# Kernel optimization log

Measured on AMD Instinct MI355X. Metric: run time of the kernel, lower is better.

## Reference

```python
import jax, jax.numpy as jnp
import numpy as np

NC, NB, NT = 512, 128, 256   # feats dims: [channels, batch, time]
H = 512                      # hidden_size
NCLS = 97                    # num_classes
NUM_STEPS = 32               # fixed decode length (= text_length.max())


def setup_inputs() -> dict:
    key = jax.random.key(0)
    ks = jax.random.split(key, 12)
    s = 1.0 / np.sqrt(H)
    inp = {
        "feats": jax.random.normal(ks[0], (NC, NB, NT), jnp.float32),
        "text_length": jnp.full((NB,), NUM_STEPS, jnp.int32),
        # AttentionCell params
        "Wi2h": jax.random.normal(ks[1], (H, NC), jnp.float32) * s,   # i2h, no bias
        "Wh2h": jax.random.normal(ks[2], (H, H), jnp.float32) * s,
        "bh2h": jax.random.normal(ks[3], (H,), jnp.float32) * s,
        "Wscore": jax.random.normal(ks[4], (1, H), jnp.float32) * s,  # score, no bias
        # GRUCell params (gate order: r, z, n as in PyTorch)
        "Wih": jax.random.normal(ks[5], (3 * H, NC), jnp.float32) * s,
        "Whh": jax.random.normal(ks[6], (3 * H, H), jnp.float32) * s,
        "bih": jax.random.normal(ks[7], (3 * H,), jnp.float32) * s,
        "bhh": jax.random.normal(ks[8], (3 * H,), jnp.float32) * s,
        # generator: Linear(hidden_size, num_classes - 1)
        "Wgen": jax.random.normal(ks[9], (NCLS - 1, H), jnp.float32) * s,
        "bgen": jax.random.normal(ks[10], (NCLS - 1,), jnp.float32) * s,
    }
    return inp


def reference(feats, text_length, Wi2h, Wh2h, bh2h, Wscore, Wih, Whh, bih, bhh, Wgen, bgen):
    # feats: [nC, nB, nT]
    nC, nB, nT = feats.shape
    # i2h(feats) is step-independent -> hoist out of the loop (same math)
    feats_proj = jnp.einsum('cbt,hc->bth', feats, Wi2h)  # [nB, nT, H]
    w_score = Wscore[0]                                   # [H]

    def step(h, _):
        # additive attention
        hp = h @ Wh2h.T + bh2h                                  # [nB, H]
        e = jnp.tanh(feats_proj + hp[:, None, :]) @ w_score     # [nB, nT]
        alpha = jax.nn.softmax(e, axis=1)                       # [nB, nT]
        context = jnp.einsum('cbt,bt->bc', feats, alpha)        # [nB, nC]
        # GRUCell(context, h), PyTorch semantics
        gi = context @ Wih.T + bih                              # [nB, 3H]
        gh = h @ Whh.T + bhh                                    # [nB, 3H]
        ir, iz, in_ = jnp.split(gi, 3, axis=1)
        hr, hz, hn = jnp.split(gh, 3, axis=1)
        r = jax.nn.sigmoid(ir + hr)
        z = jax.nn.sigmoid(iz + hz)
        n = jnp.tanh(in_ + r * hn)
        h_new = (1.0 - z) * n + z * h
        return h_new, h_new

    h0 = jnp.zeros((nB, feats_proj.shape[-1]), feats.dtype)
    _, hiddens = jax.lax.scan(step, h0, None, length=NUM_STEPS)  # [T, nB, H]
    # all lengths == NUM_STEPS -> gather is a per-batch flatten
    new_hiddens = hiddens.transpose(1, 0, 2).reshape(-1, hiddens.shape[-1])  # [nB*T, H]
    probs = new_hiddens @ Wgen.T + bgen                          # [nB*T, NCLS-1]
    return probs
```

## Files before the change

kernel.cpp:

```cpp
#include <hip/hip_runtime.h>
#include <math.h>

#define NBATCH 128
#define NTIME  256
#define NCH    512
#define NH     512
#define NSTEPS 32
#define NOUT   96
#define MTOT   32768

typedef __attribute__((ext_vector_type(8))) short short8v;
typedef __attribute__((ext_vector_type(4))) float f32x4;

__device__ __forceinline__ float fast_tanh(float x) {
    x = fminf(fmaxf(x, -30.f), 30.f);
    float u = __expf(2.f * x);
    return (u - 1.f) / (u + 1.f);
}
__device__ __forceinline__ float fast_sigmoid(float x) {
    x = fminf(fmaxf(x, -30.f), 30.f);
    return 1.f / (1.f + __expf(-x));
}
__device__ __forceinline__ float wave_reduce_sum(float s) {
    #pragma unroll
    for (int off = 32; off; off >>= 1) s += __shfl_xor(s, off, 64);
    return s;
}
__device__ __forceinline__ float wave_reduce_max(float s) {
    #pragma unroll
    for (int off = 32; off; off >>= 1) s = fmaxf(s, __shfl_xor(s, off, 64));
    return s;
}
__device__ __forceinline__ unsigned short f2bf(float f) {
    unsigned u = __builtin_bit_cast(unsigned, f);
    return (unsigned short)((u + 0x7FFFu + ((u >> 16) & 1u)) >> 16);
}
__device__ __forceinline__ float bflo(unsigned u) {
    return __builtin_bit_cast(float, u << 16);
}
__device__ __forceinline__ float bfhi(unsigned u) {
    return __builtin_bit_cast(float, u & 0xFFFF0000u);
}

__global__ __launch_bounds__(256) void k_w2bf(const float* __restrict__ W,
                                              unsigned short* __restrict__ Wb) {
    #pragma unroll
    for (int r = 0; r < 4; ++r) {
        int idx = (blockIdx.x * 256 + threadIdx.x) + r * 16384;
        float4 v = *(const float4*)(W + (size_t)idx * 4);
        ushort4 o;
        o.x = f2bf(v.x); o.y = f2bf(v.y); o.z = f2bf(v.z); o.w = f2bf(v.w);
        *(ushort4*)(Wb + (size_t)idx * 4) = o;
    }
}

__global__ __launch_bounds__(256) void k_wg2bf(const float* __restrict__ Wih,
                                               const float* __restrict__ Whh,
                                               unsigned short* __restrict__ Wgb) {
    #pragma unroll
    for (int r = 0; r < 4; ++r) {
        int idx = (blockIdx.x * 256 + threadIdx.x) + r * 98304;
        const float* src = (idx < 196608) ? (Wih + (size_t)idx * 4)
                                          : (Whh + (size_t)(idx - 196608) * 4);
        float4 v = *(const float4*)src;
        ushort4 o;
        o.x = f2bf(v.x); o.y = f2bf(v.y); o.z = f2bf(v.z); o.w = f2bf(v.w);
        *(ushort4*)(Wgb + (size_t)idx * 4) = o;
    }
}

__global__ __launch_bounds__(256) void k_feats2bf(const float* __restrict__ feats,
                                                  unsigned short* __restrict__ Fb) {
    __shared__ float tl[64][65];
    const int m0 = (blockIdx.x & 511) * 64;
    const int k0 = (blockIdx.x >> 9) * 64;
    const int tid = threadIdx.x;
    #pragma unroll
    for (int p = 0; p < 4; ++p) {
        int fid = tid + p * 256;
        int row = fid >> 4, c4 = fid & 15;
        float4 v = *(const float4*)(feats + (size_t)(k0 + row) * MTOT + m0 + c4 * 4);
        tl[row][c4 * 4 + 0] = v.x; tl[row][c4 * 4 + 1] = v.y;
        tl[row][c4 * 4 + 2] = v.z; tl[row][c4 * 4 + 3] = v.w;
    }
    __syncthreads();
    #pragma unroll
    for (int p = 0; p < 4; ++p) {
        int cid = tid + p * 256;
        int mm = cid >> 4, ch = cid & 15;
        ushort4 o;
        o.x = f2bf(tl[ch * 4 + 0][mm]);
        o.y = f2bf(tl[ch * 4 + 1][mm]);
        o.z = f2bf(tl[ch * 4 + 2][mm]);
        o.w = f2bf(tl[ch * 4 + 3][mm]);
        *(ushort4*)(Fb + (size_t)(m0 + mm) * 512 + k0 + ch * 4) = o;
    }
}

__global__ __launch_bounds__(1024) void k_fcopy(const float* __restrict__ f,
                                                unsigned short* __restrict__ o) {
    int gid = blockIdx.x * 1024 + threadIdx.x;
    float4 v = *(const float4*)(f + (size_t)gid * 4);
    ushort4 s;
    s.x = f2bf(v.x); s.y = f2bf(v.y); s.z = f2bf(v.z); s.w = f2bf(v.w);
    *(ushort4*)(o + (size_t)gid * 4) = s;
}

__global__ __launch_bounds__(256) void k_fp_mfma(const unsigned short* __restrict__ Wb,
                                                 const unsigned short* __restrict__ Fb,
                                                 unsigned short* __restrict__ fp_bf) {
    __shared__ char SB[49152];
    unsigned short* As = (unsigned short*)SB;
    unsigned short* Bs = (unsigned short*)(SB + 16384);
    float* tl = (float*)SB;
    const int m0 = (blockIdx.x & 127) * 256;
    const int h0 = (blockIdx.x >> 7) * 128;
    const int tid = threadIdx.x;
    const int lane = tid & 63, wid = tid >> 6;
    const int wh = wid & 1, wm = wid >> 1;
    f32x4 acc[4][8];
    #pragma unroll
    for (int i = 0; i < 4; ++i)
        #pragma unroll
        for (int j = 0; j < 8; ++j) acc[i][j] = (f32x4)0.f;

    for (int k0 = 0; k0 < 512; k0 += 64) {
        #pragma unroll
        for (int i = 0; i < 4; ++i) {
            int cid = tid + i * 256;
            int row = cid >> 3, ch = cid & 7;
            uint4 v = *(const uint4*)(Wb + (size_t)(h0 + row) * 512 + k0 + ch * 8);
            *(uint4*)(As + row * 64 + ((ch ^ (row & 7)) << 3)) = v;
        }
        #pragma unroll
        for (int i = 0; i < 8; ++i) {
            int cid = tid + i * 256;
            int row = cid >> 3, ch = cid & 7;
            uint4 v = *(const uint4*)(Fb + (size_t)(m0 + row) * 512 + k0 + ch * 8);
            *(uint4*)(Bs + row * 64 + ((ch ^ (row & 7)) << 3)) = v;
        }
        __syncthreads();
        #pragma unroll
        for (int ks = 0; ks < 2; ++ks) {
            short8v a[4], b[8];
            #pragma unroll
            for (int hf = 0; hf < 4; ++hf) {
                int row = wh * 64 + hf * 16 + (lane & 15);
                int ch = ks * 4 + (lane >> 4);
                a[hf] = *(const short8v*)(As + row * 64 + ((ch ^ (row & 7)) << 3));
            }
            #pragma unroll
            for (int mf = 0; mf < 8; ++mf) {
                int row = wm * 128 + mf * 16 + (lane & 15);
                int ch = ks * 4 + (lane >> 4);
                b[mf] = *(const short8v*)(Bs + row * 64 + ((ch ^ (row & 7)) << 3));
            }
            #pragma unroll
            for (int hf = 0; hf < 4; ++hf)
                #pragma unroll
                for (int mf = 0; mf < 8; ++mf)
                    acc[hf][mf] = __builtin_amdgcn_mfma_f32_16x16x32_bf16(
                        a[hf], b[mf], acc[hf][mf], 0, 0, 0);
        }
        __syncthreads();
    }
    #pragma unroll
    for (int hf = 0; hf < 4; ++hf) {
        #pragma unroll
        for (int mf = 0; mf < 8; ++mf) {
            int ml = wm * 128 + mf * 16 + (lane & 15);
            int col = wh * 16 + (lane >> 4) * 4;
            tl[ml * 33 + col + 0] = acc[hf][mf][0];
            tl[ml * 33 + col + 1] = acc[hf][mf][1];
            tl[ml * 33 + col + 2] = acc[hf][mf][2];
            tl[ml * 33 + col + 3] = acc[hf][mf][3];
        }
        __syncthreads();
        #pragma unroll
        for (int mi = 0; mi < 8; ++mi) {
            int ml = (tid >> 3) + mi * 32;
            int hl4 = (tid & 7) * 4;
            float v0 = tl[ml * 33 + hl4 + 0];
            float v1 = tl[ml * 33 + hl4 + 1];
            float v2 = tl[ml * 33 + hl4 + 2];
            float v3 = tl[ml * 33 + hl4 + 3];
            int hg = h0 + ((hl4 < 16) ? (hf * 16 + hl4) : (64 + hf * 16 + hl4 - 16));
            ushort4 o;
            o.x = f2bf(v0); o.y = f2bf(v1); o.z = f2bf(v2); o.w = f2bf(v3);
            *(ushort4*)(fp_bf + (size_t)(m0 + ml) * 512 + hg) = o;
        }
        __syncthreads();
    }
}

__global__ __launch_bounds__(256) void k_wt(const float* __restrict__ W,
                                            unsigned short* __restrict__ WTb) {
    __shared__ float tl[32][33];
    const int bi = blockIdx.x & 15, bj = blockIdx.x >> 4;
    const int tx = threadIdx.x & 31, ty8 = threadIdx.x >> 5;
    #pragma unroll
    for (int i = 0; i < 4; ++i) {
        int r = ty8 * 4 + i;
        tl[r][tx] = W[(size_t)(bj * 32 + r) * NH + bi * 32 + tx];
    }
    __syncthreads();
    #pragma unroll
    for (int i = 0; i < 4; ++i) {
        int c = ty8 * 4 + i;
        WTb[(size_t)(bi * 32 + c) * NH + bj * 32 + tx] = f2bf(tl[tx][c]);
    }
}

__global__ __launch_bounds__(1024) void k_hp0(const float* __restrict__ bh2h,
                                              float* __restrict__ hp) {
    int i = blockIdx.x * 1024 + threadIdx.x;
    hp[i] = bh2h[i & 511];
}

__global__ __launch_bounds__(512) void k_e(const unsigned short* __restrict__ fp_bf,
                                           const float* __restrict__ hp,
                                           const float* __restrict__ wscore,
                                           float* __restrict__ e) {
    const int b = blockIdx.x >> 3;
    const int t0 = (blockIdx.x & 7) * 32;
    const int tid = threadIdx.x;
    const int lane = tid & 63, w = tid >> 6;
    float4 h0 = *(const float4*)(hp + (size_t)b * NH + lane * 8);
    float4 h1 = *(const float4*)(hp + (size_t)b * NH + lane * 8 + 4);
    float4 w0 = *(const float4*)(wscore + lane * 8);
    float4 w1 = *(const float4*)(wscore + lane * 8 + 4);
    const unsigned short* base = fp_bf + (size_t)(b * NTIME + t0 + w * 4) * NH + lane * 8;
    uint4 v0 = *(const uint4*)(base);
    uint4 v1 = *(const uint4*)(base + NH);
    uint4 v2 = *(const uint4*)(base + 2 * NH);
    uint4 v3 = *(const uint4*)(base + 3 * NH);
    uint4 vv[4] = {v0, v1, v2, v3};
    #pragma unroll
    for (int it = 0; it < 4; ++it) {
        uint4 v = vv[it];
        float s = fast_tanh(bflo(v.x) + h0.x) * w0.x + fast_tanh(bfhi(v.x) + h0.y) * w0.y +
                  fast_tanh(bflo(v.y) + h0.z) * w0.z + fast_tanh(bfhi(v.y) + h0.w) * w0.w +
                  fast_tanh(bflo(v.z) + h1.x) * w1.x + fast_tanh(bfhi(v.z) + h1.y) * w1.y +
                  fast_tanh(bflo(v.w) + h1.z) * w1.z + fast_tanh(bfhi(v.w) + h1.w) * w1.w;
        s = wave_reduce_sum(s);
        if (lane == 0) e[b * NTIME + t0 + w * 4 + it] = s;
    }
}

__global__ __launch_bounds__(512) void k_ctx2(const float* __restrict__ e,
                                              const unsigned short* __restrict__ featsb,
                                              unsigned short* __restrict__ ctx_bf) {
    __shared__ float als[256];
    __shared__ float red[8];
    const int b = blockIdx.x >> 3;
    const int c0 = (blockIdx.x & 7) * 64;
    const int tid = threadIdx.x;
    const int lane = tid & 63, w = tid >> 6;
    float v = (tid < 256) ? e[b * NTIME + tid] : -3.4e38f;
    float m = wave_reduce_max(v);
    if (lane == 0) red[w] = m;
    __syncthreads();
    m = red[0];
    #pragma unroll
    for (int i = 1; i < 8; ++i) m = fmaxf(m, red[i]);
    float ex = (tid < 256) ? __expf(v - m) : 0.f;
    float s = wave_reduce_sum(ex);
    __syncthreads();
    if (lane == 0) red[w] = s;
    __syncthreads();
    s = 0.f;
    #pragma unroll
    for (int i = 0; i < 8; ++i) s += red[i];
    if (tid < 256) als[tid] = ex / s;
    __syncthreads();

    float4 al = *(const float4*)&als[lane * 4];
    #pragma unroll
    for (int cc = 0; cc < 8; ++cc) {
        int c = c0 + w * 8 + cc;
        uint2 fv = *(const uint2*)(featsb + (size_t)(c * NBATCH + b) * NTIME + lane * 4);
        float sc = bflo(fv.x) * al.x + bfhi(fv.x) * al.y +
                   bflo(fv.y) * al.z + bfhi(fv.y) * al.w;
        sc = wave_reduce_sum(sc);
        if (lane == 0) ctx_bf[(size_t)b * NCH + c] = f2bf(sc);
    }
}

__global__ __launch_bounds__(256) void k_gmfma(const unsigned short* __restrict__ ctx_bf,
                                               const unsigned short* __restrict__ h_bf,
                                               const unsigned short* __restrict__ Wgb,
                                               float* __restrict__ g2) {
    __shared__ unsigned short As[128 * 64];
    __shared__ unsigned short Bs[128 * 64];
    const int j0 = blockIdx.x * 128;
    const unsigned short* A = (j0 < 1536) ? ctx_bf : h_bf;
    const int tid = threadIdx.x;
    const int lane = tid & 63, wid = tid >> 6;
    const int wb = wid & 1, wj = wid >> 1;
    f32x4 acc[4][4];
    #pragma unroll
    for (int i = 0; i < 4; ++i)
        #pragma unroll
        for (int j = 0; j < 4; ++j) acc[i][j] = (f32x4)0.f;

    for (int k0 = 0; k0 < 512; k0 += 64) {
        #pragma unroll
        for (int i = 0; i < 4; ++i) {
            int cid = tid + i * 256;
            int row = cid >> 3, ch = cid & 7;
            uint4 va = *(const uint4*)(A + (size_t)row * 512 + k0 + ch * 8);
            *(uint4*)(As + row * 64 + ((ch ^ (row & 7)) << 3)) = va;
            uint4 vb = *(const uint4*)(Wgb + (size_t)(j0 + row) * 512 + k0 + ch * 8);
            *(uint4*)(Bs + row * 64 + ((ch ^ (row & 7)) << 3)) = vb;
        }
        __syncthreads();
        #pragma unroll
        for (int ks = 0; ks < 2; ++ks) {
            short8v a[4], b[4];
            #pragma unroll
            for (int f = 0; f < 4; ++f) {
                int rowa = wb * 64 + f * 16 + (lane & 15);
                int rowb = wj * 64 + f * 16 + (lane & 15);
                int ch = ks * 4 + (lane >> 4);
                a[f] = *(const short8v*)(As + rowa * 64 + ((ch ^ (rowa & 7)) << 3));
                b[f] = *(const short8v*)(Bs + rowb * 64 + ((ch ^ (rowb & 7)) << 3));
            }
            #pragma unroll
            for (int bf = 0; bf < 4; ++bf)
                #pragma unroll
                for (int jf = 0; jf < 4; ++jf)
                    acc[bf][jf] = __builtin_amdgcn_mfma_f32_16x16x32_bf16(
                        a[bf], b[jf], acc[bf][jf], 0, 0, 0);
        }
        __syncthreads();
    }
    #pragma unroll
    for (int bf = 0; bf < 4; ++bf) {
        int b = wb * 64 + bf * 16 + (lane >> 4) * 4;
        #pragma unroll
        for (int jf = 0; jf < 4; ++jf) {
            int j = j0 + wj * 64 + jf * 16 + (lane & 15);
            *(f32x4*)(g2 + (size_t)j * NBATCH + b) = acc[bf][jf];
        }
    }
}

__global__ __launch_bounds__(1024) void k_comb_hp(const float* __restrict__ g2,
                                                  const float* __restrict__ hprev,
                                                  float* __restrict__ hidn,
                                                  unsigned short* __restrict__ h_bf,
                                                  const float* __restrict__ bih,
                                                  const float* __restrict__ bhh,
                                                  const unsigned short* __restrict__ WTb,
                                                  const float* __restrict__ bh2h,
                                                  float* __restrict__ hp) {
    __shared__ float h_s[4 * 512];
    __shared__ float scr2[16 * 4 * 16 * 4];
    const int blk = blockIdx.x;
    const int b0 = (blk >> 3) * 4;
    const int jbase = (blk & 7) * 64;
    const int tid = threadIdx.x;
    #pragma unroll
    for (int rep = 0; rep < 2; ++rep) {
        int idx = tid + rep * 1024;
        int bi = idx & 3, kk = idx >> 2;
        int b = b0 + bi;
        float ir  = g2[(size_t)(0 * 512 + kk) * NBATCH + b] + bih[kk];
        float iz  = g2[(size_t)(1 * 512 + kk) * NBATCH + b] + bih[512 + kk];
        float in_ = g2[(size_t)(2 * 512 + kk) * NBATCH + b] + bih[1024 + kk];
        float hr  = g2[(size_t)(3 * 512 + kk) * NBATCH + b] + bhh[kk];
        float hz  = g2[(size_t)(4 * 512 + kk) * NBATCH + b] + bhh[512 + kk];
        float hn  = g2[(size_t)(5 * 512 + kk) * NBATCH + b] + bhh[1024 + kk];
        float r = fast_sigmoid(ir + hr);
        float z = fast_sigmoid(iz + hz);
        float ng = fast_tanh(in_ + r * hn);
        float hv = hprev[(size_t)b * NH + kk];
        float hnew = (1.f - z) * ng + z * hv;
        h_s[bi * 512 + kk] = hnew;
        if ((blk & 7) == 0) {
            hidn[(size_t)b * NH + kk] = hnew;
            h_bf[(size_t)b * NH + kk] = f2bf(hnew);
        }
    }
    __syncthreads();
    {
        const int jq = tid & 15, bi = (tid >> 4) & 3, kq = tid >> 6;
        const int j = jbase + jq * 4;
        float4 acc = make_float4(0.f, 0.f, 0.f, 0.f);
        #pragma unroll 8
        for (int kk = 0; kk < 32; ++kk) {
            int k = kq * 32 + kk;
            uint2 wq = *(const uint2*)(WTb + (size_t)k * NH + j);
            float hv = h_s[bi * 512 + k];
            acc.x += hv * bflo(wq.x); acc.y += hv * bfhi(wq.x);
            acc.z += hv * bflo(wq.y); acc.w += hv * bfhi(wq.y);
        }
        *(float4*)&scr2[((kq * 4 + bi) * 16 + jq) * 4] = acc;
    }
    __syncthreads();
    if (tid < 64) {
        const int bi = tid >> 4, jq = tid & 15;
        float4 sum = make_float4(0.f, 0.f, 0.f, 0.f);
        #pragma unroll
        for (int kq = 0; kq < 16; ++kq) {
            float4 p = *(const float4*)&scr2[((kq * 4 + bi) * 16 + jq) * 4];
            sum.x += p.x; sum.y += p.y; sum.z += p.z; sum.w += p.w;
        }
        int j = jbase + jq * 4;
        float4 bb = *(const float4*)(bh2h + j);
        sum.x += bb.x; sum.y += bb.y; sum.z += bb.z; sum.w += bb.w;
        *(float4*)(hp + (size_t)(b0 + bi) * NH + j) = sum;
    }
}

__global__ __launch_bounds__(256) void k_gen(const float* __restrict__ hid,
                                             const float* __restrict__ Wgen,
                                             const float* __restrict__ bgen,
                                             float* __restrict__ out) {
    __shared__ float As[32][36];
    __shared__ float Bs[32][97];
    const int m0 = blockIdx.x * 32;
    const int tid = threadIdx.x;
    const int tx = tid & 31, ty = tid >> 5;
    float acc[4][3] = {};
    for (int k0 = 0; k0 < 512; k0 += 32) {
        {
            int mm = tid >> 3, kq = (tid & 7) << 2;
            int m = m0 + mm, s = m & 31, b = m >> 5;
            float4 v = *(const float4*)(hid + (size_t)(s + 1) * 65536 + b * 512 + k0 + kq);
            *(float4*)(&As[mm][kq]) = v;
        }
        #pragma unroll
        for (int i = 0; i < 3; ++i) {
            int f4 = tid + i * 256;
            int nn = f4 >> 3, kq = (f4 & 7) << 2;
            float4 v = *(const float4*)(Wgen + (size_t)nn * 512 + k0 + kq);
            Bs[kq + 0][nn] = v.x; Bs[kq + 1][nn] = v.y;
            Bs[kq + 2][nn] = v.z; Bs[kq + 3][nn] = v.w;
        }
        __syncthreads();
        #pragma unroll
        for (int kk = 0; kk < 32; ++kk) {
            float bv[3];
            #pragma unroll
            for (int j = 0; j < 3; ++j) bv[j] = Bs[kk][tx * 3 + j];
            #pragma unroll
            for (int i = 0; i < 4; ++i) {
                float a = As[ty * 4 + i][kk];
                #pragma unroll
                for (int j = 0; j < 3; ++j) acc[i][j] += a * bv[j];
            }
        }
        __syncthreads();
    }
    #pragma unroll
    for (int i = 0; i < 4; ++i)
        #pragma unroll
        for (int j = 0; j < 3; ++j)
            out[(size_t)(m0 + ty * 4 + i) * NOUT + tx * 3 + j] = acc[i][j] + bgen[tx * 3 + j];
}

extern "C" void kernel_launch(void* const* d_in, const int* in_sizes, int n_in,
                              void* d_out, int out_size, void* d_ws, size_t ws_size,
                              hipStream_t stream) {
    const float* feats  = (const float*)d_in[0];
    const float* Wi2h   = (const float*)d_in[2];
    const float* Wh2h   = (const float*)d_in[3];
    const float* bh2h   = (const float*)d_in[4];
    const float* Wscore = (const float*)d_in[5];
    const float* Wih    = (const float*)d_in[6];
    const float* Whh    = (const float*)d_in[7];
    const float* bih    = (const float*)d_in[8];
    const float* bhh    = (const float*)d_in[9];
    const float* Wgen   = (const float*)d_in[10];
    const float* bgen   = (const float*)d_in[11];
    float* out = (float*)d_out;

    float* ws  = (float*)d_ws;
    unsigned short* fp_bf  = (unsigned short*)ws;
    float*          hid    = ws + 8388608;
    float*          hpctx  = hid + 2162688;
    unsigned short* ctx_bf = (unsigned short*)(hpctx + 65536);
    unsigned short* h_bf   = (unsigned short*)(hpctx + 65536 + 32768);
    unsigned short* WTb    = (unsigned short*)(hpctx + 65536 + 65536);
    unsigned short* Wgb    = (unsigned short*)(hpctx + 65536 + 65536 + 131072);
    unsigned short* Wb     = (unsigned short*)(hpctx + 65536 + 65536 + 131072 + 786432);
    unsigned short* Fb     = (unsigned short*)(hpctx + 65536 + 65536 + 131072 + 786432 + 131072);
    unsigned short* featsb = Fb;

    float* e  = out;
    float* g2 = out;

    hipMemsetAsync(hid, 0, 65536 * sizeof(float), stream);
    hipMemsetAsync(h_bf, 0, 65536 * sizeof(unsigned short), stream);
    k_wt<<<256, 256, 0, stream>>>(Wh2h, WTb);
    k_w2bf<<<64, 256, 0, stream>>>(Wi2h, Wb);
    k_wg2bf<<<384, 256, 0, stream>>>(Wih, Whh, Wgb);
    k_feats2bf<<<4096, 256, 0, stream>>>(feats, Fb);
    k_fp_mfma<<<512, 256, 0, stream>>>(Wb, Fb, fp_bf);
    k_fcopy<<<4096, 1024, 0, stream>>>(feats, featsb);
    k_hp0<<<64, 1024, 0, stream>>>(bh2h, hpctx);

    for (int s = 0; s < NSTEPS; ++s) {
        const float* h = hid + (size_t)s * 65536;
        float* hn      = hid + (size_t)(s + 1) * 65536;
        k_e<<<1024, 512, 0, stream>>>(fp_bf, hpctx, Wscore, e);
        k_ctx2<<<1024, 512, 0, stream>>>(e, featsb, ctx_bf);
        k_gmfma<<<24, 256, 0, stream>>>(ctx_bf, h_bf, Wgb, g2);
        k_comb_hp<<<256, 1024, 0, stream>>>(g2, h, hn, h_bf, bih, bhh, WTb, bh2h, hpctx);
    }
    k_gen<<<128, 256, 0, stream>>>(hid, Wgen, bgen, out);
}
```

Baseline: 1.564 ms.

## Use direct global-to-LDS loads in MFMA GEMMs and fuse feats conversions

The two bf16 MFMA GEMM kernels now stage their A/B tiles with global_load_lds 16-byte direct loads, with the swizzle applied on the source address, so data no longer passes through VGPRs. When the workspace is large enough, the two feats conversion passes (transposed bf16 copy and straight bf16 copy) are fused into one kernel that reads feats once and writes both buffers to separate regions. This removes a full extra read of the 64MB feats tensor and one launch. It depends on the workspace size check and on the LDS layout produced by the direct loads matching the existing swizzled reads.

```diff
diff --git a/kernel.cpp b/kernel.cpp
--- a/kernel.cpp
+++ b/kernel.cpp
@@ -11,6 +11,13 @@
 
 typedef __attribute__((ext_vector_type(8))) short short8v;
 typedef __attribute__((ext_vector_type(4))) float f32x4;
+
+typedef const __attribute__((address_space(1))) unsigned int g_as_uint;
+typedef __attribute__((address_space(3))) unsigned int l_as_uint;
+
+__device__ __forceinline__ void gl_lds16(const void* g, void* l) {
+    __builtin_amdgcn_global_load_lds((g_as_uint*)g, (l_as_uint*)l, 16, 0, 0);
+}
 
 __device__ __forceinline__ float fast_tanh(float x) {
     x = fminf(fmaxf(x, -30.f), 30.f);
@@ -69,8 +76,9 @@
     }
 }
 
-__global__ __launch_bounds__(256) void k_feats2bf(const float* __restrict__ feats,
-                                                  unsigned short* __restrict__ Fb) {
+__global__ __launch_bounds__(256) void k_prep(const float* __restrict__ feats,
+                                              unsigned short* __restrict__ featsb,
+                                              unsigned short* __restrict__ Fb) {
     __shared__ float tl[64][65];
     const int m0 = (blockIdx.x & 511) * 64;
     const int k0 = (blockIdx.x >> 9) * 64;
@@ -82,6 +90,9 @@
         float4 v = *(const float4*)(feats + (size_t)(k0 + row) * MTOT + m0 + c4 * 4);
         tl[row][c4 * 4 + 0] = v.x; tl[row][c4 * 4 + 1] = v.y;
         tl[row][c4 * 4 + 2] = v.z; tl[row][c4 * 4 + 3] = v.w;
+        ushort4 o;
+        o.x = f2bf(v.x); o.y = f2bf(v.y); o.z = f2bf(v.z); o.w = f2bf(v.w);
+        *(ushort4*)(featsb + (size_t)(k0 + row) * MTOT + m0 + c4 * 4) = o;
     }
     __syncthreads();
     #pragma unroll
@@ -97,6 +108,34 @@
     }
 }
 
+__global__ __launch_bounds__(256) void k_feats2bf(const float* __restrict__ feats,
+                                                  unsigned short* __restrict__ Fb) {
+    __shared__ float tl[64][65];
+    const int m0 = (blockIdx.x & 511) * 64;
+    const int k0 = (blockIdx.x >> 9) * 64;
+    const int tid = threadIdx.x;
+    #pragma unroll
+    for (int p = 0; p < 4; ++p) {
+        int fid = tid + p * 256;
+        int row = fid >> 4, c4 = fid & 15;
+        float4 v = *(const float4*)(feats + (size_t)(k0 + row) * MTOT + m0 + c4 * 4);
+        tl[row][c4 * 4 + 0] = v.x; tl[row][c4 * 4 + 1] = v.y;
+        tl[row][c4 * 4 + 2] = v.z; tl[row][c4 * 4 + 3] = v.w;
+    }
+    __syncthreads();
+    #pragma unroll
+    for (int p = 0; p < 4; ++p) {
+        int cid = tid + p * 256;
+        int mm = cid >> 4, ch = cid & 15;
+        ushort4 o;
+        o.x = f2bf(tl[ch * 4 + 0][mm]);
+        o.y = f2bf(tl[ch * 4 + 1][mm]);
+        o.z = f2bf(tl[ch * 4 + 2][mm]);
+        o.w = f2bf(tl[ch * 4 + 3][mm]);
+        *(ushort4*)(Fb + (size_t)(m0 + mm) * 512 + k0 + ch * 4) = o;
+    }
+}
+
 __global__ __launch_bounds__(1024) void k_fcopy(const float* __restrict__ f,
                                                 unsigned short* __restrict__ o) {
     int gid = blockIdx.x * 1024 + threadIdx.x;
@@ -116,8 +155,10 @@
     const int m0 = (blockIdx.x & 127) * 256;
     const int h0 = (blockIdx.x >> 7) * 128;
     const int tid = threadIdx.x;
-    const int lane = tid & 63, wid = tid >> 6;
+    const int lane = tid & 63;
+    const int wid = __builtin_amdgcn_readfirstlane(tid >> 6);
     const int wh = wid & 1, wm = wid >> 1;
+    const int l8 = lane >> 3, c8 = lane & 7;
     f32x4 acc[4][8];
     #pragma unroll
     for (int i = 0; i < 4; ++i)
@@ -127,17 +168,17 @@
     for (int k0 = 0; k0 < 512; k0 += 64) {
         #pragma unroll
         for (int i = 0; i < 4; ++i) {
-            int cid = tid + i * 256;
-            int row = cid >> 3, ch = cid & 7;
-            uint4 v = *(const uint4*)(Wb + (size_t)(h0 + row) * 512 + k0 + ch * 8);
-            *(uint4*)(As + row * 64 + ((ch ^ (row & 7)) << 3)) = v;
+            int slot = wid * 4 + i;
+            int row = slot * 8 + l8;
+            gl_lds16(Wb + (size_t)(h0 + row) * 512 + k0 + ((c8 ^ (row & 7)) << 3),
+                     As + slot * 512);
         }
         #pragma unroll
         for (int i = 0; i < 8; ++i) {
-            int cid = tid + i * 256;
-            int row = cid >> 3, ch = cid & 7;
-            uint4 v = *(const uint4*)(Fb + (size_t)(m0 + row) * 512 + k0 + ch * 8);
-            *(uint4*)(Bs + row * 64 + ((ch ^ (row & 7)) << 3)) = v;
+            int slot = wid * 8 + i;
+            int row = slot * 8 + l8;
+            gl_lds16(Fb + (size_t)(m0 + row) * 512 + k0 + ((c8 ^ (row & 7)) << 3),
+                     Bs + slot * 512);
         }
         __syncthreads();
         #pragma unroll
@@ -295,8 +336,10 @@
     const int j0 = blockIdx.x * 128;
     const unsigned short* A = (j0 < 1536) ? ctx_bf : h_bf;
     const int tid = threadIdx.x;
-    const int lane = tid & 63, wid = tid >> 6;
+    const int lane = tid & 63;
+    const int wid = __builtin_amdgcn_readfirstlane(tid >> 6);
     const int wb = wid & 1, wj = wid >> 1;
+    const int l8 = lane >> 3, c8 = lane & 7;
     f32x4 acc[4][4];
     #pragma unroll
     for (int i = 0; i < 4; ++i)
@@ -306,12 +349,11 @@
     for (int k0 = 0; k0 < 512; k0 += 64) {
         #pragma unroll
         for (int i = 0; i < 4; ++i) {
-            int cid = tid + i * 256;
-            int row = cid >> 3, ch = cid & 7;
-            uint4 va = *(const uint4*)(A + (size_t)row * 512 + k0 + ch * 8);
-            *(uint4*)(As + row * 64 + ((ch ^ (row & 7)) << 3)) = va;
-            uint4 vb = *(const uint4*)(Wgb + (size_t)(j0 + row) * 512 + k0 + ch * 8);
-            *(uint4*)(Bs + row * 64 + ((ch ^ (row & 7)) << 3)) = vb;
+            int slot = wid * 4 + i;
+            int row = slot * 8 + l8;
+            int src_off = (c8 ^ (row & 7)) << 3;
+            gl_lds16(A + (size_t)row * 512 + k0 + src_off, As + slot * 512);
+            gl_lds16(Wgb + (size_t)(j0 + row) * 512 + k0 + src_off, Bs + slot * 512);
         }
         __syncthreads();
         #pragma unroll
@@ -486,7 +528,9 @@
     unsigned short* Wgb    = (unsigned short*)(hpctx + 65536 + 65536 + 131072);
     unsigned short* Wb     = (unsigned short*)(hpctx + 65536 + 65536 + 131072 + 786432);
     unsigned short* Fb     = (unsigned short*)(hpctx + 65536 + 65536 + 131072 + 786432 + 131072);
-    unsigned short* featsb = Fb;
+    const size_t base_floats = 8388608 + 2162688 + 65536 + 32768 + 32768 + 131072 + 786432 + 131072 + 8388608;
+    const bool big = ws_size >= (base_floats + 8388608) * sizeof(float);
+    unsigned short* featsb = big ? (Fb + 16777216) : Fb;
 
     float* e  = out;
     float* g2 = out;
@@ -496,9 +540,14 @@
     k_wt<<<256, 256, 0, stream>>>(Wh2h, WTb);
     k_w2bf<<<64, 256, 0, stream>>>(Wi2h, Wb);
     k_wg2bf<<<384, 256, 0, stream>>>(Wih, Whh, Wgb);
-    k_feats2bf<<<4096, 256, 0, stream>>>(feats, Fb);
-    k_fp_mfma<<<512, 256, 0, stream>>>(Wb, Fb, fp_bf);
-    k_fcopy<<<4096, 1024, 0, stream>>>(feats, featsb);
+    if (big) {
+        k_prep<<<4096, 256, 0, stream>>>(feats, featsb, Fb);
+        k_fp_mfma<<<512, 256, 0, stream>>>(Wb, Fb, fp_bf);
+    } else {
+        k_feats2bf<<<4096, 256, 0, stream>>>(feats, Fb);
+        k_fp_mfma<<<512, 256, 0, stream>>>(Wb, Fb, fp_bf);
+        k_fcopy<<<4096, 1024, 0, stream>>>(feats, featsb);
+    }
     k_hp0<<<64, 1024, 0, stream>>>(bh2h, hpctx);
 
     for (int s = 0; s < NSTEPS; ++s) {
```

Result: no change. 1.567 ms (median of 2 runs) (+0.2%).
